# Optimization experiments

Measured on AMD Instinct MI355X. Metric: run time of the kernel, lower is better.

Reference implementation:

```python
import jax, jax.numpy as jnp
import numpy as np

B, C, H, W = 8, 512, 64, 64
D = C // 8  # 64

def setup_inputs() -> dict:
    key = jax.random.key(0)
    ks = jax.random.split(key, 10)
    s = 0.02
    return {
        "x":  jax.random.normal(ks[0], (B, C, H, W), dtype=jnp.float32),
        "Wq": jax.random.normal(ks[1], (D, C), dtype=jnp.float32) * s,
        "bq": jnp.zeros((D,), dtype=jnp.float32),
        "Wk": jax.random.normal(ks[2], (D, C), dtype=jnp.float32) * s,
        "bk": jnp.zeros((D,), dtype=jnp.float32),
        "Wv": jax.random.normal(ks[3], (D, C), dtype=jnp.float32) * s,
        "bv": jnp.zeros((D,), dtype=jnp.float32),
        "Wo": jax.random.normal(ks[4], (C, D), dtype=jnp.float32) * s,
        "bo": jnp.zeros((C,), dtype=jnp.float32),
        "gamma": jnp.full((1,), 0.5, dtype=jnp.float32),
    }

def reference(x, Wq, bq, Wk, bk, Wv, bv, Wo, bo, gamma):
    b, c, h, w = x.shape
    n = h * w
    xf = x.reshape(b, c, n)                                   # (B, C, N)
    # 1x1 convs == channel matmuls (spectral_norm only reparametrizes the weight)
    q = jnp.einsum('dc,bcn->bnd', Wq, xf) + bq                # (B, N, D)
    k = jnp.einsum('dc,bcn->bdn', Wk, xf) + bk[:, None]       # (B, D, N)
    v = jnp.einsum('dc,bcn->bdn', Wv, xf) + bv[:, None]       # (B, D, N)
    # unscaled scores, softmax over key index (last dim)
    attn = jax.nn.softmax(jnp.einsum('bnd,bdm->bnm', q, k), axis=-1)  # (B, N, N)
    out = jnp.einsum('bdm,bnm->bdn', v, attn)                 # (B, D, N)
    out = jnp.einsum('cd,bdn->bcn', Wo, out) + bo[:, None]    # (B, C, N)
    return (out * gamma + xf).reshape(b, c, h, w)
```

## Files before the change

kernel.cpp:

```cpp
#include <hip/hip_runtime.h>
#include <hip/hip_bf16.h>

#define DEVFN __device__ __forceinline__

typedef __bf16 bf16x8 __attribute__((ext_vector_type(8)));
typedef float f32x4 __attribute__((ext_vector_type(4)));
typedef float float4_t __attribute__((ext_vector_type(4)));
typedef unsigned short ushort8_t __attribute__((ext_vector_type(8)));
typedef unsigned short ushort4_t __attribute__((ext_vector_type(4)));
typedef unsigned int uint4_t __attribute__((ext_vector_type(4)));

constexpr int Bd = 8, Cd = 512, Nd = 4096, Dd = 64;

DEVFN unsigned short f2bf(float f) {
    union { float f; unsigned int u; } v; v.f = f;
    unsigned int r = (v.u + 0x7FFFu + ((v.u >> 16) & 1u)) >> 16;
    return (unsigned short)r;
}

DEVFN unsigned int pack2(float a, float b) {
    __hip_bfloat162 h = __float22bfloat162_rn(make_float2(a, b));
    union { __hip_bfloat162 h; unsigned int u; } c; c.h = h;
    return c.u;
}

DEVFN bf16x8 ld_bf8(const unsigned short* p) {
    ushort8_t u = *(const ushort8_t*)p;
    return __builtin_bit_cast(bf16x8, u);
}

DEVFN f32x4 mfma16(bf16x8 a, bf16x8 b, f32x4 c) {
    return __builtin_amdgcn_mfma_f32_16x16x32_bf16(a, b, c, 0, 0, 0);
}

__global__ __launch_bounds__(256) void k_cvtw(
    const float* __restrict__ Wq, const float* __restrict__ Wk,
    const float* __restrict__ Wv, const float* __restrict__ Wo,
    unsigned short* __restrict__ w4)
{
    int i = blockIdx.x * 256 + threadIdx.x;
    w4[i]          = f2bf(Wq[i]);
    w4[32768 + i]  = f2bf(Wk[i]);
    w4[65536 + i]  = f2bf(Wv[i]);
    w4[98304 + i]  = f2bf(Wo[i]);
}

__global__ __launch_bounds__(128, 2) void k_qkv(
    const float* __restrict__ x,
    const unsigned short* __restrict__ wq,
    const unsigned short* __restrict__ wk,
    const unsigned short* __restrict__ wv,
    const float* __restrict__ bq, const float* __restrict__ bk, const float* __restrict__ bv,
    unsigned short* __restrict__ q_nd, unsigned short* __restrict__ k_nd,
    unsigned short* __restrict__ v_dn)
{
    const int b   = blockIdx.y;
    const int n0  = blockIdx.x * 32;
    const int tid = threadIdx.x, wid = tid >> 6, l = tid & 63;
    const int lo  = l & 15, hi = l >> 4;
    const float* xb = x + (size_t)b * Cd * Nd;

    __shared__ unsigned short smem[2][32][72];

    f32x4 acc[12] = {};

    const int scr = tid >> 3;
    const int snf = tid & 7;
    float4_t xrA[4], xrB[4];

    auto gloadA = [&](int t) {
        const int c0 = t * 64;
        #pragma unroll
        for (int p = 0; p < 4; ++p)
            xrA[p] = *(const float4_t*)(xb + (size_t)(c0 + p*16 + scr) * Nd + n0 + snf*4);
    };
    auto gloadB = [&](int t) {
        const int c0 = t * 64;
        #pragma unroll
        for (int p = 0; p < 4; ++p)
            xrB[p] = *(const float4_t*)(xb + (size_t)(c0 + p*16 + scr) * Nd + n0 + snf*4);
    };
    auto dswriteA = [&](int buf) {
        #pragma unroll
        for (int p = 0; p < 4; ++p)
            #pragma unroll
            for (int i = 0; i < 4; ++i)
                smem[buf][snf*4 + i][p*16 + scr] = f2bf(xrA[p][i]);
    };
    auto dswriteB = [&](int buf) {
        #pragma unroll
        for (int p = 0; p < 4; ++p)
            #pragma unroll
            for (int i = 0; i < 4; ++i)
                smem[buf][snf*4 + i][p*16 + scr] = f2bf(xrB[p][i]);
    };
    auto compute = [&](int buf, int t) {
        const int c0 = t * 64;
        #pragma unroll
        for (int kk = 0; kk < 2; ++kk) {
            bf16x8 af = ld_bf8(&smem[buf][wid*16 + lo][kk*32 + hi*8]);
            #pragma unroll
            for (int j = 0; j < 12; ++j) {
                const unsigned short* wm = (j < 4) ? wq : (j < 8) ? wk : wv;
                const int d0 = (j & 3) * 16;
                bf16x8 bf = ld_bf8(wm + (d0 + lo) * Cd + c0 + kk*32 + hi*8);
                acc[j] = mfma16(af, bf, acc[j]);
            }
        }
    };

    gloadA(0);
    dswriteA(0);
    gloadB(1);
    __syncthreads();
    for (int t = 0; t < 8; t += 2) {
        if (t + 2 < 8) gloadA(t + 2);
        __builtin_amdgcn_sched_barrier(0);
        compute(0, t);
        dswriteB(1);
        __syncthreads();
        if (t + 3 < 8) gloadB(t + 3);
        __builtin_amdgcn_sched_barrier(0);
        compute(1, t + 1);
        if (t + 2 < 8) dswriteA(0);
        __syncthreads();
    }

    unsigned short* tl = &smem[1][wid*16][0];
    #pragma unroll
    for (int m = 0; m < 2; ++m) {
        const float* bias = m ? bk : bq;
        #pragma unroll
        for (int jj = 0; jj < 4; ++jj) {
            const float bia = bias[jj*16 + lo];
            #pragma unroll
            for (int r = 0; r < 4; ++r)
                tl[(hi*4 + r) * 72 + jj*16 + lo] = f2bf(acc[m*4 + jj][r] + bia);
        }
        asm volatile("" ::: "memory");
        const int row = l >> 2, dg = l & 3;
        ushort8_t a0 = *(const ushort8_t*)&tl[row*72 + dg*16];
        ushort8_t a1 = *(const ushort8_t*)&tl[row*72 + dg*16 + 8];
        unsigned short* dst = (m ? k_nd : q_nd)
            + ((size_t)b * Nd + n0 + wid*16 + row) * 64 + dg*16;
        *(ushort8_t*)dst = a0; *(ushort8_t*)(dst + 8) = a1;
        asm volatile("" ::: "memory");
    }

    unsigned short* vt = &smem[0][0][0];
    #pragma unroll
    for (int jj = 0; jj < 4; ++jj) {
        const float bia = bv[jj*16 + lo];
        #pragma unroll
        for (int r = 0; r < 4; ++r)
            vt[(jj*16 + lo) * 36 + wid*16 + hi*4 + r] = f2bf(acc[8 + jj][r] + bia);
    }
    __syncthreads();
    #pragma unroll
    for (int p = 0; p < 2; ++p) {
        const int d = p*32 + (tid >> 2), ng = tid & 3;
        ushort4_t a0 = *(const ushort4_t*)&vt[d*36 + ng*8];
        ushort4_t a1 = *(const ushort4_t*)&vt[d*36 + ng*8 + 4];
        unsigned short* dst = v_dn + ((size_t)b * Dd + d) * Nd + n0 + ng*8;
        *(ushort4_t*)dst = a0; *(ushort4_t*)(dst + 4) = a1;
    }
}

__global__ __launch_bounds__(256, 2) void k_attn(
    const unsigned short* __restrict__ q_nd,
    const unsigned short* __restrict__ k_nd,
    const unsigned short* __restrict__ v_dn,
    unsigned short* __restrict__ o_nd)
{
    const int bid = blockIdx.x;
    const int b   = bid & 7;
    const int n0  = (bid >> 3) * 64;
    const int tid = threadIdx.x, wid = tid >> 6, l = tid & 63;
    const int lo  = l & 15, hi = l >> 4;
    const int lsw = lo & 7;
    const int qh  = wid >> 1;
    const int kh  = wid & 1;
    const int wk0 = kh * 32;

    __shared__ unsigned short k_tiles[2][64 * 64];
    __shared__ unsigned short v_tiles[2][64 * 64];
    __shared__ float red_acc[2][2][4][256];
    __shared__ float red_l[2][2][16];

    const unsigned short* qb = q_nd + (size_t)b * Nd * Dd;
    const unsigned short* kb = k_nd + (size_t)b * Nd * Dd;
    const unsigned short* vb = v_dn + (size_t)b * Dd * Nd;

    bf16x8 aq[2][2];
    #pragma unroll
    for (int qs = 0; qs < 2; ++qs)
        #pragma unroll
        for (int kc = 0; kc < 2; ++kc)
            aq[qs][kc] = ld_bf8(qb + (size_t)(n0 + qh*32 + qs*16 + lo) * 64 + kc*32 + hi*8);

    f32x4 acc[2][4] = {};
    float l_p[2] = {0.f, 0.f};

    const int sr = tid >> 3, ss = tid & 7;
    const int kwsl = (ss ^ (sr & 7)) * 8;
    const int vkh = ss >> 2, vsl = ss & 3, vms = vsl >> 1;
    const int vg0 = vkh * 4 + ((2 * vsl) & 3);
    const int vg1 = vkh * 4 + ((2 * vsl + 1) & 3);
    const int vsw = sr & 7;
    ushort8_t kr0, kr1, vr0, vr1;

    auto gload = [&](int t) {
        const size_t m1 = (size_t)t * 64;
        kr0 = *(const ushort8_t*)(kb + (m1 + sr) * 64 + ss * 8);
        kr1 = *(const ushort8_t*)(kb + (m1 + 32 + sr) * 64 + ss * 8);
        vr0 = *(const ushort8_t*)(vb + (size_t)sr * Nd + m1 + ss * 8);
        vr1 = *(const ushort8_t*)(vb + (size_t)(32 + sr) * Nd + m1 + ss * 8);
    };
    auto dswrite = [&](int buf) {
        unsigned short* kt = k_tiles[buf];
        unsigned short* vt = v_tiles[buf];
        *(ushort8_t*)(kt + sr * 64 + kwsl)        = kr0;
        *(ushort8_t*)(kt + (32 + sr) * 64 + kwsl) = kr1;
        ushort4_t a0 = __builtin_shufflevector(vr0, vr0, 0, 1, 2, 3);
        ushort4_t a1 = __builtin_shufflevector(vr0, vr0, 4, 5, 6, 7);
        ushort4_t b0 = __builtin_shufflevector(vr1, vr1, 0, 1, 2, 3);
        ushort4_t b1 = __builtin_shufflevector(vr1, vr1, 4, 5, 6, 7);
        *(ushort4_t*)(vt + sr * 64 + (vg0 ^ vsw) * 8 + vms * 4)        = a0;
        *(ushort4_t*)(vt + sr * 64 + (vg1 ^ vsw) * 8 + vms * 4)        = a1;
        *(ushort4_t*)(vt + (32 + sr) * 64 + (vg0 ^ vsw) * 8 + vms * 4) = b0;
        *(ushort4_t*)(vt + (32 + sr) * 64 + (vg1 ^ vsw) * 8 + vms * 4) = b1;
    };

    auto compute = [&](int buf) {
        const unsigned short* kt = k_tiles[buf];
        const unsigned short* vt = v_tiles[buf];
        f32x4 s[2][2] = {};
        #pragma unroll
        for (int ms = 0; ms < 2; ++ms) {
            #pragma unroll
            for (int kc = 0; kc < 2; ++kc) {
                bf16x8 kf = ld_bf8(kt + (wk0 + ms*16 + lo) * 64 + (((kc*4 + hi) ^ lsw) * 8));
                #pragma unroll
                for (int qs = 0; qs < 2; ++qs)
                    s[qs][ms] = mfma16(kf, aq[qs][kc], s[qs][ms]);
            }
        }
        bf16x8 vf[4];
        #pragma unroll
        for (int ds = 0; ds < 4; ++ds)
            vf[ds] = ld_bf8(vt + (ds*16 + lo) * 64 + (((kh*4 + hi) ^ lsw) * 8));
        #pragma unroll
        for (int qs = 0; qs < 2; ++qs) {
            float p[2][4];
            #pragma unroll
            for (int ms = 0; ms < 2; ++ms)
                #pragma unroll
                for (int r = 0; r < 4; ++r)
                    p[ms][r] = __expf(s[qs][ms][r]);
            l_p[qs] += ((p[0][0] + p[0][1]) + (p[0][2] + p[0][3]))
                     + ((p[1][0] + p[1][1]) + (p[1][2] + p[1][3]));
            uint4_t w;
            w[0] = pack2(p[0][0], p[0][1]);
            w[1] = pack2(p[0][2], p[0][3]);
            w[2] = pack2(p[1][0], p[1][1]);
            w[3] = pack2(p[1][2], p[1][3]);
            bf16x8 apf = __builtin_bit_cast(bf16x8, w);
            #pragma unroll
            for (int ds = 0; ds < 4; ++ds)
                acc[qs][ds] = mfma16(apf, vf[ds], acc[qs][ds]);
        }
    };

    constexpr int NT = Nd / 64;
    gload(0);
    dswrite(0);
    __syncthreads();
    for (int t = 0; t < NT; ++t) {
        const int cur = t & 1;
        if (t + 1 < NT) gload(t + 1);
        __builtin_amdgcn_sched_barrier(0);
        compute(cur);
        if (t + 1 < NT) dswrite(cur ^ 1);
        __syncthreads();
    }

    float lh[2];
    #pragma unroll
    for (int qs = 0; qs < 2; ++qs) {
        float ps = l_p[qs];
        ps += __shfl_xor(ps, 16, 64);
        ps += __shfl_xor(ps, 32, 64);
        lh[qs] = ps;
    }
    if (kh == 1) {
        #pragma unroll
        for (int qs = 0; qs < 2; ++qs) {
            #pragma unroll
            for (int ds = 0; ds < 4; ++ds)
                *(f32x4*)&red_acc[qh][qs][ds][l * 4] = acc[qs][ds];
            red_l[qh][qs][lo] = lh[qs];
        }
    }
    __syncthreads();
    if (kh == 0) {
        #pragma unroll
        for (int qs = 0; qs < 2; ++qs) {
            #pragma unroll
            for (int ds = 0; ds < 4; ++ds)
                acc[qs][ds] += *(const f32x4*)&red_acc[qh][qs][ds][l * 4];
            float l_tot = lh[qs] + red_l[qh][qs][lo];
            #pragma unroll
            for (int r = 0; r < 4; ++r) {
                float lq = __shfl(l_tot, hi * 4 + r, 16);
                float rl = 1.0f / lq;
                #pragma unroll
                for (int ds = 0; ds < 4; ++ds) {
                    float o = acc[qs][ds][r] * rl;
                    o_nd[((size_t)b * Nd + n0 + qh*32 + qs*16 + hi*4 + r) * 64 + ds*16 + lo] = f2bf(o);
                }
            }
        }
    }
}

__global__ __launch_bounds__(256) void k_oproj(
    const unsigned short* __restrict__ o_nd,
    const unsigned short* __restrict__ wo,
    const float* __restrict__ bo,
    const float* __restrict__ gamma,
    const float* __restrict__ x,
    float* __restrict__ out)
{
    const int b   = blockIdx.y;
    const int n0  = blockIdx.x * 64;
    const int tid = threadIdx.x, wid = tid >> 6, l = tid & 63;
    const int lo  = l & 15, hi = l >> 4;
    const int n0w = n0 + wid * 16;
    const float g = gamma[0];

    bf16x8 ao[2];
    #pragma unroll
    for (int kc = 0; kc < 2; ++kc)
        ao[kc] = ld_bf8(o_nd + ((size_t)b * Nd + n0w + lo) * 64 + kc*32 + hi*8);

    for (int ct = 0; ct < 32; ++ct) {
        f32x4 acc = {};
        #pragma unroll
        for (int kc = 0; kc < 2; ++kc) {
            bf16x8 bw = ld_bf8(wo + (ct*16 + lo) * 64 + kc*32 + hi*8);
            acc = mfma16(ao[kc], bw, acc);
        }
        const int c = ct*16 + lo;
        const float bc = bo[c];
        const size_t base = ((size_t)b * Cd + c) * Nd + n0w + hi*4;
        float4_t xv = *(const float4_t*)(x + base);
        float4_t ov;
        #pragma unroll
        for (int r = 0; r < 4; ++r) ov[r] = g * (acc[r] + bc) + xv[r];
        *(float4_t*)(out + base) = ov;
    }
}

extern "C" void kernel_launch(void* const* d_in, const int* in_sizes, int n_in,
                              void* d_out, int out_size, void* d_ws, size_t ws_size,
                              hipStream_t stream) {
    (void)in_sizes; (void)n_in; (void)out_size; (void)ws_size;
    const float* x  = (const float*)d_in[0];
    const float* Wq = (const float*)d_in[1];
    const float* bq = (const float*)d_in[2];
    const float* Wk = (const float*)d_in[3];
    const float* bk = (const float*)d_in[4];
    const float* Wv = (const float*)d_in[5];
    const float* bv = (const float*)d_in[6];
    const float* Wo = (const float*)d_in[7];
    const float* bo = (const float*)d_in[8];
    const float* gm = (const float*)d_in[9];
    float* out = (float*)d_out;

    unsigned short* w4   = (unsigned short*)d_ws;
    unsigned short* q_nd = w4 + 131072;
    unsigned short* k_nd = q_nd + (size_t)Bd * Nd * Dd;
    unsigned short* v_dn = k_nd + (size_t)Bd * Nd * Dd;
    unsigned short* o_nd = v_dn + (size_t)Bd * Nd * Dd;

    k_cvtw<<<128, 256, 0, stream>>>(Wq, Wk, Wv, Wo, w4);
    dim3 gq(Nd / 32, Bd);
    k_qkv<<<gq, 128, 0, stream>>>(x, w4, w4 + 32768, w4 + 65536, bq, bk, bv, q_nd, k_nd, v_dn);
    k_attn<<<512, 256, 0, stream>>>(q_nd, k_nd, v_dn, o_nd);
    dim3 g1(Nd / 64, Bd);
    k_oproj<<<g1, 256, 0, stream>>>(o_nd, w4 + 98304, bo, gm, x, out);
}
```

Baseline: 144.1 us.

## Split attention block across 8 waves with 16 query rows each

The attention kernel now runs 512 threads (8 waves) per block instead of 256. Each wave handles 16 query rows instead of 32, and each thread loads one K row chunk and one V row chunk per tile instead of two. The intent is to halve per-wave register use and raise occupancy so exp and LDS latency are better hidden. In exchange, each K/V fragment read from LDS feeds half as many MFMAs, which increases LDS traffic per unit of compute.

```diff
diff --git a/kernel.cpp b/kernel.cpp
--- a/kernel.cpp
+++ b/kernel.cpp
@@ -166,7 +166,7 @@
     }
 }
 
-__global__ __launch_bounds__(256, 2) void k_attn(
+__global__ __launch_bounds__(512, 4) void k_attn(
     const unsigned short* __restrict__ q_nd,
     const unsigned short* __restrict__ k_nd,
     const unsigned short* __restrict__ v_dn,
@@ -184,22 +184,20 @@
 
     __shared__ unsigned short k_tiles[2][64 * 64];
     __shared__ unsigned short v_tiles[2][64 * 64];
-    __shared__ float red_acc[2][2][4][256];
-    __shared__ float red_l[2][2][16];
+    __shared__ float red_acc[4][4][256];
+    __shared__ float red_l[4][16];
 
     const unsigned short* qb = q_nd + (size_t)b * Nd * Dd;
     const unsigned short* kb = k_nd + (size_t)b * Nd * Dd;
     const unsigned short* vb = v_dn + (size_t)b * Dd * Nd;
 
-    bf16x8 aq[2][2];
-    #pragma unroll
-    for (int qs = 0; qs < 2; ++qs)
-        #pragma unroll
-        for (int kc = 0; kc < 2; ++kc)
-            aq[qs][kc] = ld_bf8(qb + (size_t)(n0 + qh*32 + qs*16 + lo) * 64 + kc*32 + hi*8);
-
-    f32x4 acc[2][4] = {};
-    float l_p[2] = {0.f, 0.f};
+    bf16x8 aq[2];
+    #pragma unroll
+    for (int kc = 0; kc < 2; ++kc)
+        aq[kc] = ld_bf8(qb + (size_t)(n0 + qh*16 + lo) * 64 + kc*32 + hi*8);
+
+    f32x4 acc[4] = {};
+    float l_p = 0.f;
 
     const int sr = tid >> 3, ss = tid & 7;
     const int kwsl = (ss ^ (sr & 7)) * 8;
@@ -207,68 +205,56 @@
     const int vg0 = vkh * 4 + ((2 * vsl) & 3);
     const int vg1 = vkh * 4 + ((2 * vsl + 1) & 3);
     const int vsw = sr & 7;
-    ushort8_t kr0, kr1, vr0, vr1;
+    ushort8_t kr, vr;
 
     auto gload = [&](int t) {
         const size_t m1 = (size_t)t * 64;
-        kr0 = *(const ushort8_t*)(kb + (m1 + sr) * 64 + ss * 8);
-        kr1 = *(const ushort8_t*)(kb + (m1 + 32 + sr) * 64 + ss * 8);
-        vr0 = *(const ushort8_t*)(vb + (size_t)sr * Nd + m1 + ss * 8);
-        vr1 = *(const ushort8_t*)(vb + (size_t)(32 + sr) * Nd + m1 + ss * 8);
+        kr = *(const ushort8_t*)(kb + (m1 + sr) * 64 + ss * 8);
+        vr = *(const ushort8_t*)(vb + (size_t)sr * Nd + m1 + ss * 8);
     };
     auto dswrite = [&](int buf) {
         unsigned short* kt = k_tiles[buf];
         unsigned short* vt = v_tiles[buf];
-        *(ushort8_t*)(kt + sr * 64 + kwsl)        = kr0;
-        *(ushort8_t*)(kt + (32 + sr) * 64 + kwsl) = kr1;
-        ushort4_t a0 = __builtin_shufflevector(vr0, vr0, 0, 1, 2, 3);
-        ushort4_t a1 = __builtin_shufflevector(vr0, vr0, 4, 5, 6, 7);
-        ushort4_t b0 = __builtin_shufflevector(vr1, vr1, 0, 1, 2, 3);
-        ushort4_t b1 = __builtin_shufflevector(vr1, vr1, 4, 5, 6, 7);
-        *(ushort4_t*)(vt + sr * 64 + (vg0 ^ vsw) * 8 + vms * 4)        = a0;
-        *(ushort4_t*)(vt + sr * 64 + (vg1 ^ vsw) * 8 + vms * 4)        = a1;
-        *(ushort4_t*)(vt + (32 + sr) * 64 + (vg0 ^ vsw) * 8 + vms * 4) = b0;
-        *(ushort4_t*)(vt + (32 + sr) * 64 + (vg1 ^ vsw) * 8 + vms * 4) = b1;
+        *(ushort8_t*)(kt + sr * 64 + kwsl) = kr;
+        ushort4_t a0 = __builtin_shufflevector(vr, vr, 0, 1, 2, 3);
+        ushort4_t a1 = __builtin_shufflevector(vr, vr, 4, 5, 6, 7);
+        *(ushort4_t*)(vt + sr * 64 + (vg0 ^ vsw) * 8 + vms * 4) = a0;
+        *(ushort4_t*)(vt + sr * 64 + (vg1 ^ vsw) * 8 + vms * 4) = a1;
     };
 
     auto compute = [&](int buf) {
         const unsigned short* kt = k_tiles[buf];
         const unsigned short* vt = v_tiles[buf];
-        f32x4 s[2][2] = {};
+        f32x4 s[2] = {};
         #pragma unroll
         for (int ms = 0; ms < 2; ++ms) {
             #pragma unroll
             for (int kc = 0; kc < 2; ++kc) {
                 bf16x8 kf = ld_bf8(kt + (wk0 + ms*16 + lo) * 64 + (((kc*4 + hi) ^ lsw) * 8));
-                #pragma unroll
-                for (int qs = 0; qs < 2; ++qs)
-                    s[qs][ms] = mfma16(kf, aq[qs][kc], s[qs][ms]);
+                s[ms] = mfma16(kf, aq[kc], s[ms]);
             }
         }
         bf16x8 vf[4];
         #pragma unroll
         for (int ds = 0; ds < 4; ++ds)
             vf[ds] = ld_bf8(vt + (ds*16 + lo) * 64 + (((kh*4 + hi) ^ lsw) * 8));
-        #pragma unroll
-        for (int qs = 0; qs < 2; ++qs) {
-            float p[2][4];
-            #pragma unroll
-            for (int ms = 0; ms < 2; ++ms)
-                #pragma unroll
-                for (int r = 0; r < 4; ++r)
-                    p[ms][r] = __expf(s[qs][ms][r]);
-            l_p[qs] += ((p[0][0] + p[0][1]) + (p[0][2] + p[0][3]))
-                     + ((p[1][0] + p[1][1]) + (p[1][2] + p[1][3]));
-            uint4_t w;
-            w[0] = pack2(p[0][0], p[0][1]);
-            w[1] = pack2(p[0][2], p[0][3]);
-            w[2] = pack2(p[1][0], p[1][1]);
-            w[3] = pack2(p[1][2], p[1][3]);
-            bf16x8 apf = __builtin_bit_cast(bf16x8, w);
-            #pragma unroll
-            for (int ds = 0; ds < 4; ++ds)
-                acc[qs][ds] = mfma16(apf, vf[ds], acc[qs][ds]);
-        }
+        float p[2][4];
+        #pragma unroll
+        for (int ms = 0; ms < 2; ++ms)
+            #pragma unroll
+            for (int r = 0; r < 4; ++r)
+                p[ms][r] = __expf(s[ms][r]);
+        l_p += ((p[0][0] + p[0][1]) + (p[0][2] + p[0][3]))
+             + ((p[1][0] + p[1][1]) + (p[1][2] + p[1][3]));
+        uint4_t w;
+        w[0] = pack2(p[0][0], p[0][1]);
+        w[1] = pack2(p[0][2], p[0][3]);
+        w[2] = pack2(p[1][0], p[1][1]);
+        w[3] = pack2(p[1][2], p[1][3]);
+        bf16x8 apf = __builtin_bit_cast(bf16x8, w);
+        #pragma unroll
+        for (int ds = 0; ds < 4; ++ds)
+            acc[ds] = mfma16(apf, vf[ds], acc[ds]);
     };
 
     constexpr int NT = Nd / 64;
@@ -284,40 +270,29 @@
         __syncthreads();
     }
 
-    float lh[2];
-    #pragma unroll
-    for (int qs = 0; qs < 2; ++qs) {
-        float ps = l_p[qs];
-        ps += __shfl_xor(ps, 16, 64);
-        ps += __shfl_xor(ps, 32, 64);
-        lh[qs] = ps;
-    }
+    float lh = l_p;
+    lh += __shfl_xor(lh, 16, 64);
+    lh += __shfl_xor(lh, 32, 64);
     if (kh == 1) {
         #pragma unroll
-        for (int qs = 0; qs < 2; ++qs) {
-            #pragma unroll
-            for (int ds = 0; ds < 4; ++ds)
-                *(f32x4*)&red_acc[qh][qs][ds][l * 4] = acc[qs][ds];
-            red_l[qh][qs][lo] = lh[qs];
-        }
+        for (int ds = 0; ds < 4; ++ds)
+            *(f32x4*)&red_acc[qh][ds][l * 4] = acc[ds];
+        red_l[qh][lo] = lh;
     }
     __syncthreads();
     if (kh == 0) {
         #pragma unroll
-        for (int qs = 0; qs < 2; ++qs) {
-            #pragma unroll
-            for (int ds = 0; ds < 4; ++ds)
-                acc[qs][ds] += *(const f32x4*)&red_acc[qh][qs][ds][l * 4];
-            float l_tot = lh[qs] + red_l[qh][qs][lo];
-            #pragma unroll
-            for (int r = 0; r < 4; ++r) {
-                float lq = __shfl(l_tot, hi * 4 + r, 16);
-                float rl = 1.0f / lq;
-                #pragma unroll
-                for (int ds = 0; ds < 4; ++ds) {
-                    float o = acc[qs][ds][r] * rl;
-                    o_nd[((size_t)b * Nd + n0 + qh*32 + qs*16 + hi*4 + r) * 64 + ds*16 + lo] = f2bf(o);
-                }
+        for (int ds = 0; ds < 4; ++ds)
+            acc[ds] += *(const f32x4*)&red_acc[qh][ds][l * 4];
+        float l_tot = lh + red_l[qh][lo];
+        #pragma unroll
+        for (int r = 0; r < 4; ++r) {
+            float lq = __shfl(l_tot, hi * 4 + r, 16);
+            float rl = 1.0f / lq;
+            #pragma unroll
+            for (int ds = 0; ds < 4; ++ds) {
+                float o = acc[ds][r] * rl;
+                o_nd[((size_t)b * Nd + n0 + qh*16 + hi*4 + r) * 64 + ds*16 + lo] = f2bf(o);
             }
         }
     }
@@ -386,7 +361,7 @@
     k_cvtw<<<128, 256, 0, stream>>>(Wq, Wk, Wv, Wo, w4);
     dim3 gq(Nd / 32, Bd);
     k_qkv<<<gq, 128, 0, stream>>>(x, w4, w4 + 32768, w4 + 65536, bq, bk, bv, q_nd, k_nd, v_dn);
-    k_attn<<<512, 256, 0, stream>>>(q_nd, k_nd, v_dn, o_nd);
+    k_attn<<<512, 512, 0, stream>>>(q_nd, k_nd, v_dn, o_nd);
     dim3 g1(Nd / 64, Bd);
     k_oproj<<<g1, 256, 0, stream>>>(o_nd, w4 + 98304, bo, gm, x, out);
 }
```

Result: no change. 146.4 us (+1.5%).

## Split attention key loop across 8 waves with two tiles per iteration

Applied to the files above, without the earlier changes.

The attention kernel grows from 256 to 512 threads. The extra wave pairs each handle a second 64-key tile, so every iteration stages 128 keys and the loop runs half as many times. Partial accumulators from the four key-groups are reduced through LDS, reusing the K/V tile buffers to save shared memory. This trades more waves per block and a larger final reduction for fewer barriers per key, and it demands tighter register budgets under the new launch bounds.

```diff
diff --git a/kernel.cpp b/kernel.cpp
--- a/kernel.cpp
+++ b/kernel.cpp
@@ -166,7 +166,7 @@
     }
 }
 
-__global__ __launch_bounds__(256, 2) void k_attn(
+__global__ __launch_bounds__(512, 4) void k_attn(
     const unsigned short* __restrict__ q_nd,
     const unsigned short* __restrict__ k_nd,
     const unsigned short* __restrict__ v_dn,
@@ -178,14 +178,13 @@
     const int tid = threadIdx.x, wid = tid >> 6, l = tid & 63;
     const int lo  = l & 15, hi = l >> 4;
     const int lsw = lo & 7;
-    const int qh  = wid >> 1;
-    const int kh  = wid & 1;
+    const int qh  = wid >> 2;
+    const int kh  = (wid >> 1) & 1;
+    const int tp  = wid & 1;
     const int wk0 = kh * 32;
 
-    __shared__ unsigned short k_tiles[2][64 * 64];
-    __shared__ unsigned short v_tiles[2][64 * 64];
-    __shared__ float red_acc[2][2][4][256];
-    __shared__ float red_l[2][2][16];
+    __shared__ __align__(16) unsigned short kv_lds[2][2][2][64 * 64];
+    __shared__ float red_l[3][2][2][16];
 
     const unsigned short* qb = q_nd + (size_t)b * Nd * Dd;
     const unsigned short* kb = k_nd + (size_t)b * Nd * Dd;
@@ -209,31 +208,33 @@
     const int vsw = sr & 7;
     ushort8_t kr0, kr1, vr0, vr1;
 
-    auto gload = [&](int t) {
-        const size_t m1 = (size_t)t * 64;
+    auto gload = [&](int it) {
+        const size_t m1 = (size_t)it * 128;
         kr0 = *(const ushort8_t*)(kb + (m1 + sr) * 64 + ss * 8);
-        kr1 = *(const ushort8_t*)(kb + (m1 + 32 + sr) * 64 + ss * 8);
+        kr1 = *(const ushort8_t*)(kb + (m1 + 64 + sr) * 64 + ss * 8);
         vr0 = *(const ushort8_t*)(vb + (size_t)sr * Nd + m1 + ss * 8);
-        vr1 = *(const ushort8_t*)(vb + (size_t)(32 + sr) * Nd + m1 + ss * 8);
+        vr1 = *(const ushort8_t*)(vb + (size_t)sr * Nd + m1 + 64 + ss * 8);
     };
     auto dswrite = [&](int buf) {
-        unsigned short* kt = k_tiles[buf];
-        unsigned short* vt = v_tiles[buf];
-        *(ushort8_t*)(kt + sr * 64 + kwsl)        = kr0;
-        *(ushort8_t*)(kt + (32 + sr) * 64 + kwsl) = kr1;
+        unsigned short* kt0 = &kv_lds[0][buf][0][0];
+        unsigned short* kt1 = &kv_lds[0][buf][1][0];
+        unsigned short* vt0 = &kv_lds[1][buf][0][0];
+        unsigned short* vt1 = &kv_lds[1][buf][1][0];
+        *(ushort8_t*)(kt0 + sr * 64 + kwsl) = kr0;
+        *(ushort8_t*)(kt1 + sr * 64 + kwsl) = kr1;
         ushort4_t a0 = __builtin_shufflevector(vr0, vr0, 0, 1, 2, 3);
         ushort4_t a1 = __builtin_shufflevector(vr0, vr0, 4, 5, 6, 7);
         ushort4_t b0 = __builtin_shufflevector(vr1, vr1, 0, 1, 2, 3);
         ushort4_t b1 = __builtin_shufflevector(vr1, vr1, 4, 5, 6, 7);
-        *(ushort4_t*)(vt + sr * 64 + (vg0 ^ vsw) * 8 + vms * 4)        = a0;
-        *(ushort4_t*)(vt + sr * 64 + (vg1 ^ vsw) * 8 + vms * 4)        = a1;
-        *(ushort4_t*)(vt + (32 + sr) * 64 + (vg0 ^ vsw) * 8 + vms * 4) = b0;
-        *(ushort4_t*)(vt + (32 + sr) * 64 + (vg1 ^ vsw) * 8 + vms * 4) = b1;
+        *(ushort4_t*)(vt0 + sr * 64 + (vg0 ^ vsw) * 8 + vms * 4) = a0;
+        *(ushort4_t*)(vt0 + sr * 64 + (vg1 ^ vsw) * 8 + vms * 4) = a1;
+        *(ushort4_t*)(vt1 + sr * 64 + (vg0 ^ vsw) * 8 + vms * 4) = b0;
+        *(ushort4_t*)(vt1 + sr * 64 + (vg1 ^ vsw) * 8 + vms * 4) = b1;
     };
 
     auto compute = [&](int buf) {
-        const unsigned short* kt = k_tiles[buf];
-        const unsigned short* vt = v_tiles[buf];
+        const unsigned short* kt = &kv_lds[0][buf][tp][0];
+        const unsigned short* vt = &kv_lds[1][buf][tp][0];
         f32x4 s[2][2] = {};
         #pragma unroll
         for (int ms = 0; ms < 2; ++ms) {
@@ -271,16 +272,16 @@
         }
     };
 
-    constexpr int NT = Nd / 64;
+    constexpr int NIT = Nd / 128;
     gload(0);
     dswrite(0);
     __syncthreads();
-    for (int t = 0; t < NT; ++t) {
-        const int cur = t & 1;
-        if (t + 1 < NT) gload(t + 1);
+    for (int it = 0; it < NIT; ++it) {
+        const int cur = it & 1;
+        if (it + 1 < NIT) gload(it + 1);
         __builtin_amdgcn_sched_barrier(0);
         compute(cur);
-        if (t + 1 < NT) dswrite(cur ^ 1);
+        if (it + 1 < NIT) dswrite(cur ^ 1);
         __syncthreads();
     }
 
@@ -292,26 +293,35 @@
         ps += __shfl_xor(ps, 32, 64);
         lh[qs] = ps;
     }
-    if (kh == 1) {
+    float* red = (float*)&kv_lds[0][0][0][0];
+    const int g = (kh * 2 + tp) - 1;
+    if (g >= 0) {
         #pragma unroll
         for (int qs = 0; qs < 2; ++qs) {
             #pragma unroll
-            for (int ds = 0; ds < 4; ++ds)
-                *(f32x4*)&red_acc[qh][qs][ds][l * 4] = acc[qs][ds];
-            red_l[qh][qs][lo] = lh[qs];
+            for (int ds = 0; ds < 4; ++ds) {
+                const int idx = ((g * 2 + qh) * 2 + qs) * 4 + ds;
+                *(f32x4*)&red[idx * 256 + l * 4] = acc[qs][ds];
+            }
+            red_l[g][qh][qs][lo] = lh[qs];
         }
     }
     __syncthreads();
-    if (kh == 0) {
+    if (g < 0) {
         #pragma unroll
         for (int qs = 0; qs < 2; ++qs) {
             #pragma unroll
-            for (int ds = 0; ds < 4; ++ds)
-                acc[qs][ds] += *(const f32x4*)&red_acc[qh][qs][ds][l * 4];
-            float l_tot = lh[qs] + red_l[qh][qs][lo];
+            for (int gg = 0; gg < 3; ++gg) {
+                #pragma unroll
+                for (int ds = 0; ds < 4; ++ds) {
+                    const int idx = ((gg * 2 + qh) * 2 + qs) * 4 + ds;
+                    acc[qs][ds] += *(const f32x4*)&red[idx * 256 + l * 4];
+                }
+                lh[qs] += red_l[gg][qh][qs][lo];
+            }
             #pragma unroll
             for (int r = 0; r < 4; ++r) {
-                float lq = __shfl(l_tot, hi * 4 + r, 16);
+                float lq = __shfl(lh[qs], hi * 4 + r, 16);
                 float rl = 1.0f / lq;
                 #pragma unroll
                 for (int ds = 0; ds < 4; ++ds) {
@@ -386,7 +396,7 @@
     k_cvtw<<<128, 256, 0, stream>>>(Wq, Wk, Wv, Wo, w4);
     dim3 gq(Nd / 32, Bd);
     k_qkv<<<gq, 128, 0, stream>>>(x, w4, w4 + 32768, w4 + 65536, bq, bk, bv, q_nd, k_nd, v_dn);
-    k_attn<<<512, 256, 0, stream>>>(q_nd, k_nd, v_dn, o_nd);
+    k_attn<<<512, 512, 0, stream>>>(q_nd, k_nd, v_dn, o_nd);
     dim3 g1(Nd / 64, Bd);
     k_oproj<<<g1, 256, 0, stream>>>(o_nd, w4 + 98304, bo, gm, x, out);
 }
```

Result: no change. 142.5 us (-1.1%).
